# Performance work log

Measured on AMD Instinct MI355X. Metric: run time of the kernel, lower is better.

## Reference

```python
import jax, jax.numpy as jnp
from jax import lax
import numpy as np

CH = 512      # ch_in = c_in = c_out
P = 8         # p: channels per group
NG = CH // P  # depthwise groups
PG = CH // P  # pointwise groups
EPS = 1e-5
DN = ('NCHW', 'OIHW', 'NCHW')


def leaky(x):
    return jnp.where(x >= 0, x, 0.01 * x)  # LeakyReLU default slope


def setup_inputs() -> dict:
    key = jax.random.key(0)
    ks = jax.random.split(key, 8)
    N, H, W = 16, 64, 64
    return {
        'style_encoding': jax.random.normal(ks[0], (N, 512, 4, 4), jnp.float32),
        'content_in': jax.random.normal(ks[1], (N, CH, H, W), jnp.float32),
        'dw_w': jax.random.normal(ks[2], (P, 512, 2, 2), jnp.float32) * 0.05,
        'dw_b': jax.random.normal(ks[3], (P,), jnp.float32) * 0.05,
        'pk_w': jax.random.normal(ks[4], (P, 512), jnp.float32) * 0.05,
        'pk_b': jax.random.normal(ks[5], (P,), jnp.float32) * 0.05,
        'pb_w': jax.random.normal(ks[6], (CH, 512), jnp.float32) * 0.05,
        'pb_b': jax.random.normal(ks[7], (CH,), jnp.float32) * 0.05,
    }


def reference(style_encoding, content_in, dw_w, dw_b, pk_w, pk_b, pb_w, pb_b):
    N, _, H, W = content_in.shape
    # --- KernelPredictor ---
    # depthwise kernels: 2x2 valid conv on 4x4 style map -> [N, P, 3, 3]
    d = lax.conv_general_dilated(style_encoding, dw_w, (1, 1), 'VALID',
                                 dimension_numbers=DN)
    d = leaky(d + dw_b[None, :, None, None])  # [N, P, 3, 3]
    # expand: same [P,3,3] filter for every output channel -> [N, CH, P, 3, 3]
    depthwise = jnp.broadcast_to(d[:, None], (N, CH, P, 3, 3))
    # avg-pool 4 on 4x4 style map == global mean -> [N, 512]
    s_d = jnp.mean(style_encoding, axis=(2, 3))
    pk = jnp.einsum('nc,oc->no', s_d, pk_w) + pk_b       # [N, P]  (1x1 conv)
    bias = jnp.einsum('nc,oc->no', s_d, pb_w) + pb_b     # [N, CH] (1x1 conv)

    # --- per-sample grouped convs, batched by folding batch into groups ---
    padded = jnp.pad(content_in, ((0, 0), (0, 0), (1, 1), (1, 1)), mode='reflect')
    xr = padded.reshape(1, N * CH, H + 2, W + 2)
    wr = depthwise.reshape(N * CH, P, 3, 3)
    depth = lax.conv_general_dilated(xr, wr, (1, 1), 'VALID',
                                     feature_group_count=N * NG,
                                     dimension_numbers=DN)
    depth = depth.reshape(N, CH, H, W)

    # pointwise 1x1 grouped conv: weight [N, CH, P, 1, 1], identical over out
    # channels within a sample (expand); groups = PG, CH//PG == P out ch/group
    depth_g = depth.reshape(N, PG, P, H, W)
    pw_g = jnp.broadcast_to(pk[:, None, None, :], (N, PG, P, P))  # [n,g,o,j]
    out = jnp.einsum('ngjhw,ngoj->ngohw', depth_g, pw_g).reshape(N, CH, H, W)
    predicted = leaky(out + bias[:, :, None, None])

    # --- instance-norm of content (AdaIN calc_mean_std, unbiased var) ---
    mean = jnp.mean(content_in, axis=(2, 3), keepdims=True)
    std = jnp.sqrt(jnp.var(content_in, axis=(2, 3), keepdims=True, ddof=1) + EPS)
    normalized = (content_in - mean) / std
    return normalized * predicted
```

## Files before the change

### kernel.cpp

```cpp
#include <hip/hip_runtime.h>
#include <math.h>

#define CH 512
#define P 8
#define PLANE 4096
#define EPS 1e-5f

typedef float f4 __attribute__((ext_vector_type(4)));

__device__ __forceinline__ float leaky(float x) { return x >= 0.f ? x : 0.01f * x; }

__device__ __forceinline__ float wave_sum(float v) {
    #pragma unroll
    for (int off = 32; off; off >>= 1) v += __shfl_xor(v, off, 64);
    return v;
}

__global__ __launch_bounds__(64) void sd_pk_kernel(
    const float* __restrict__ style,
    const float* __restrict__ pk_w,
    const float* __restrict__ pk_b,
    float* __restrict__ sd_out,
    float* __restrict__ S_out)
{
    const int n = blockIdx.x;
    const int lane = threadIdx.x;
    const float4* sp = (const float4*)(style + (size_t)n * 8192);
    float sd[8];
    #pragma unroll
    for (int i = 0; i < 8; ++i) {
        int c = lane + 64 * i;
        float4 a = sp[c * 4 + 0], b = sp[c * 4 + 1];
        float4 d = sp[c * 4 + 2], e = sp[c * 4 + 3];
        float s = a.x + a.y + a.z + a.w + b.x + b.y + b.z + b.w
                + d.x + d.y + d.z + d.w + e.x + e.y + e.z + e.w;
        sd[i] = s * (1.f / 16.f);
        sd_out[n * 512 + c] = sd[i];
    }
    float Ssum = 0.f;
    #pragma unroll
    for (int o = 0; o < 8; ++o) {
        float acc = 0.f;
        #pragma unroll
        for (int i = 0; i < 8; ++i)
            acc += pk_w[o * 512 + lane + 64 * i] * sd[i];
        Ssum += wave_sum(acc) + pk_b[o];
    }
    if (lane == 0) S_out[n] = Ssum;
}

__global__ __launch_bounds__(256) void dconv_kernel(
    const float* __restrict__ style,
    const float* __restrict__ dw_w,
    const float* __restrict__ dw_b,
    float* __restrict__ d_pred)
{
    const int W = blockIdx.x * 4 + (threadIdx.x >> 6);
    const int lane = threadIdx.x & 63;
    const int n = W / 72, r = W % 72;
    const int j = r / 9, pos = r % 9, y = pos / 3, x = pos % 3;
    const float* sb = style + (size_t)n * 8192;
    const float4* wp = (const float4*)dw_w;
    float acc = 0.f;
    #pragma unroll
    for (int i = 0; i < 8; ++i) {
        int c = lane + 64 * i;
        float4 w = wp[j * 512 + c];
        const float* s = sb + c * 16 + y * 4 + x;
        acc += s[0] * w.x + s[1] * w.y + s[4] * w.z + s[5] * w.w;
    }
    acc = wave_sum(acc);
    if (lane == 0) d_pred[n * 72 + r] = leaky(acc + dw_b[j]);
}

__global__ __launch_bounds__(256) void bias_kernel(
    const float* __restrict__ sd,
    const float* __restrict__ pb_w,
    const float* __restrict__ pb_b,
    float* __restrict__ bias_out)
{
    const int c = blockIdx.x * 4 + (threadIdx.x >> 6);
    const int lane = threadIdx.x & 63;
    float w[8];
    #pragma unroll
    for (int i = 0; i < 8; ++i) w[i] = pb_w[(size_t)c * 512 + lane + 64 * i];
    float acc[16];
    #pragma unroll
    for (int nn = 0; nn < 16; ++nn) acc[nn] = 0.f;
    #pragma unroll
    for (int i = 0; i < 8; ++i) {
        #pragma unroll
        for (int nn = 0; nn < 16; ++nn)
            acc[nn] += w[i] * sd[nn * 512 + lane + 64 * i];
    }
    #pragma unroll
    for (int nn = 0; nn < 16; ++nn) acc[nn] = wave_sum(acc[nn]);
    if (lane == 0) {
        float bb = pb_b[c];
        #pragma unroll
        for (int nn = 0; nn < 16; ++nn) bias_out[nn * 512 + c] = acc[nn] + bb;
    }
}

__global__ __launch_bounds__(256) void stats_kernel(
    const float* __restrict__ content,
    float* __restrict__ mean_out,
    float* __restrict__ rstd_out)
{
    const int nc = blockIdx.x;
    const int t = threadIdx.x;
    const float4* base = (const float4*)(content + (size_t)nc * PLANE);
    float s = 0.f, sq = 0.f;
    #pragma unroll
    for (int k = 0; k < 4; ++k) {
        float4 v = base[k * 256 + t];
        s  += v.x + v.y + v.z + v.w;
        sq += v.x * v.x + v.y * v.y + v.z * v.z + v.w * v.w;
    }
    #pragma unroll
    for (int off = 32; off > 0; off >>= 1) {
        s  += __shfl_down(s, off, 64);
        sq += __shfl_down(sq, off, 64);
    }
    __shared__ float ls[4], lq[4];
    const int wave = t >> 6, lane = t & 63;
    if (lane == 0) { ls[wave] = s; lq[wave] = sq; }
    __syncthreads();
    if (t == 0) {
        float S = ls[0] + ls[1] + ls[2] + ls[3];
        float Q = lq[0] + lq[1] + lq[2] + lq[3];
        float m = S * (1.f / 4096.f);
        float var = (Q - 4096.f * m * m) * (1.f / 4095.f);
        mean_out[nc] = m;
        rstd_out[nc] = rsqrtf(var + EPS);
    }
}

__global__ __launch_bounds__(256) void main_kernel(
    const float* __restrict__ content,
    const float* __restrict__ d_pred,
    const float* __restrict__ S_in,
    const float* __restrict__ bias_in,
    const float* __restrict__ mean_in,
    const float* __restrict__ rstd_in,
    float* __restrict__ out)
{
    const int b    = blockIdx.x;
    const int tile = b & 3;
    const int g    = (b >> 2) & 63;
    const int n    = b >> 8;
    const int t  = threadIdx.x;
    const int tx = t & 15, ty = t >> 4;
    const int h  = tile * 16 + ty;
    const int x0 = tx * 4;

    __shared__ float s_d[72];
    __shared__ float s_S;
    __shared__ float s_bias[8], s_mean[8], s_rstd[8];
    if (t < 72) s_d[t] = d_pred[n * 72 + t];
    if (t == 80) s_S = S_in[n];
    if (t >= 88 && t < 96) {
        int o = t - 88;
        int c = n * 512 + g * 8 + o;
        s_bias[o] = bias_in[c];
        s_mean[o] = mean_in[c];
        s_rstd[o] = rstd_in[c];
    }
    __syncthreads();

    const float* cbase = content + (size_t)(n * 512 + g * 8) * PLANE;
    float D0 = 0.f, D1 = 0.f, D2 = 0.f, D3 = 0.f;
    float4 xc[8];

    #pragma unroll
    for (int j = 0; j < 8; ++j) {
        const float* cj = cbase + j * PLANE;
        #pragma unroll
        for (int r = 0; r < 3; ++r) {
            int y = h - 1 + r;
            int ry = y < 0 ? 1 : (y > 63 ? 62 : y);
            float4 v = *(const float4*)(cj + ry * 64 + x0);
            float lv = __shfl_up(v.w, 1, 64);
            float rv = __shfl_down(v.x, 1, 64);
            float xm = (tx == 0)  ? v.y : lv;
            float xp = (tx == 15) ? v.z : rv;
            const float w0 = s_d[j * 9 + r * 3 + 0];
            const float w1 = s_d[j * 9 + r * 3 + 1];
            const float w2 = s_d[j * 9 + r * 3 + 2];
            D0 += w0 * xm  + w1 * v.x + w2 * v.y;
            D1 += w0 * v.x + w1 * v.y + w2 * v.z;
            D2 += w0 * v.y + w1 * v.z + w2 * v.w;
            D3 += w0 * v.z + w1 * v.w + w2 * xp;
            if (r == 1) xc[j] = v;
        }
    }

    const float S = s_S;
    const float P0 = D0 * S, P1 = D1 * S, P2 = D2 * S, P3 = D3 * S;
    float* obase = out + (size_t)(n * 512 + g * 8) * PLANE + h * 64 + x0;
    #pragma unroll
    for (int o = 0; o < 8; ++o) {
        float bb = s_bias[o], m = s_mean[o], rs = s_rstd[o];
        f4 res;
        res.x = (xc[o].x - m) * rs * leaky(P0 + bb);
        res.y = (xc[o].y - m) * rs * leaky(P1 + bb);
        res.z = (xc[o].z - m) * rs * leaky(P2 + bb);
        res.w = (xc[o].w - m) * rs * leaky(P3 + bb);
        __builtin_nontemporal_store(res, (f4*)(obase + o * PLANE));
    }
}

extern "C" void kernel_launch(void* const* d_in, const int* in_sizes, int n_in,
                              void* d_out, int out_size, void* d_ws, size_t ws_size,
                              hipStream_t stream) {
    const float* style   = (const float*)d_in[0];
    const float* content = (const float*)d_in[1];
    const float* dw_w    = (const float*)d_in[2];
    const float* dw_b    = (const float*)d_in[3];
    const float* pk_w    = (const float*)d_in[4];
    const float* pk_b    = (const float*)d_in[5];
    const float* pb_w    = (const float*)d_in[6];
    const float* pb_b    = (const float*)d_in[7];
    float* out = (float*)d_out;
    float* ws  = (float*)d_ws;

    const int N = 16;
    float* sd_ws   = ws;
    float* d_pred  = sd_ws + N * 512;
    float* S_ws    = d_pred + N * 72;
    float* bias_ws = S_ws + N;
    float* mean_ws = bias_ws + N * 512;
    float* rstd_ws = mean_ws + N * 512;

    sd_pk_kernel<<<N, 64, 0, stream>>>(style, pk_w, pk_b, sd_ws, S_ws);
    dconv_kernel<<<N * 72 / 4, 256, 0, stream>>>(style, dw_w, dw_b, d_pred);
    bias_kernel<<<512 / 4, 256, 0, stream>>>(sd_ws, pb_w, pb_b, bias_ws);
    stats_kernel<<<N * 512, 256, 0, stream>>>(content, mean_ws, rstd_ws);
    main_kernel<<<N * 64 * 4, 256, 0, stream>>>(content, d_pred, S_ws, bias_ws,
                                                mean_ws, rstd_ws, out);
}
```

Measured before the change: 276.8 us.

## Fuse instance-norm statistics into main kernel with per-group blocks

Removes the separate stats kernel and computes per-channel mean and rstd inside the main kernel, with each block now covering a full 8-channel group across all four row tiles. The group's content is read once for statistics and then re-read for the convolution, with the re-read expected to hit cache instead of DRAM. The cost is four times fewer blocks and a serial tile loop per block, which lowers parallelism and latency hiding.

```diff
diff --git a/kernel.cpp b/kernel.cpp
--- a/kernel.cpp
+++ b/kernel.cpp
@@ -102,111 +102,100 @@
     }
 }
 
-__global__ __launch_bounds__(256) void stats_kernel(
-    const float* __restrict__ content,
-    float* __restrict__ mean_out,
-    float* __restrict__ rstd_out)
-{
-    const int nc = blockIdx.x;
-    const int t = threadIdx.x;
-    const float4* base = (const float4*)(content + (size_t)nc * PLANE);
-    float s = 0.f, sq = 0.f;
-    #pragma unroll
-    for (int k = 0; k < 4; ++k) {
-        float4 v = base[k * 256 + t];
-        s  += v.x + v.y + v.z + v.w;
-        sq += v.x * v.x + v.y * v.y + v.z * v.z + v.w * v.w;
-    }
-    #pragma unroll
-    for (int off = 32; off > 0; off >>= 1) {
-        s  += __shfl_down(s, off, 64);
-        sq += __shfl_down(sq, off, 64);
-    }
-    __shared__ float ls[4], lq[4];
-    const int wave = t >> 6, lane = t & 63;
-    if (lane == 0) { ls[wave] = s; lq[wave] = sq; }
-    __syncthreads();
-    if (t == 0) {
-        float S = ls[0] + ls[1] + ls[2] + ls[3];
-        float Q = lq[0] + lq[1] + lq[2] + lq[3];
-        float m = S * (1.f / 4096.f);
-        float var = (Q - 4096.f * m * m) * (1.f / 4095.f);
-        mean_out[nc] = m;
-        rstd_out[nc] = rsqrtf(var + EPS);
-    }
-}
-
 __global__ __launch_bounds__(256) void main_kernel(
     const float* __restrict__ content,
     const float* __restrict__ d_pred,
     const float* __restrict__ S_in,
     const float* __restrict__ bias_in,
-    const float* __restrict__ mean_in,
-    const float* __restrict__ rstd_in,
     float* __restrict__ out)
 {
-    const int b    = blockIdx.x;
-    const int tile = b & 3;
-    const int g    = (b >> 2) & 63;
-    const int n    = b >> 8;
+    const int b = blockIdx.x;
+    const int g = b & 63, n = b >> 6;
     const int t  = threadIdx.x;
     const int tx = t & 15, ty = t >> 4;
-    const int h  = tile * 16 + ty;
     const int x0 = tx * 4;
+    const int wave = t >> 6, lane = t & 63;
 
     __shared__ float s_d[72];
     __shared__ float s_S;
     __shared__ float s_bias[8], s_mean[8], s_rstd[8];
+
     if (t < 72) s_d[t] = d_pred[n * 72 + t];
     if (t == 80) s_S = S_in[n];
     if (t >= 88 && t < 96) {
         int o = t - 88;
-        int c = n * 512 + g * 8 + o;
-        s_bias[o] = bias_in[c];
-        s_mean[o] = mean_in[c];
-        s_rstd[o] = rstd_in[c];
+        s_bias[o] = bias_in[n * 512 + g * 8 + o];
+    }
+
+    const float* cbase = content + (size_t)(n * 512 + g * 8) * PLANE;
+
+    #pragma unroll
+    for (int jj = 0; jj < 2; ++jj) {
+        const int j = wave * 2 + jj;
+        const f4* p = (const f4*)(cbase + j * PLANE);
+        float s = 0.f, q = 0.f;
+        #pragma unroll 4
+        for (int k = 0; k < 16; ++k) {
+            f4 v = p[lane + 64 * k];
+            s += v.x + v.y + v.z + v.w;
+            q += v.x * v.x + v.y * v.y + v.z * v.z + v.w * v.w;
+        }
+        #pragma unroll
+        for (int off = 32; off; off >>= 1) {
+            s += __shfl_xor(s, off, 64);
+            q += __shfl_xor(q, off, 64);
+        }
+        if (lane == 0) {
+            float m = s * (1.f / 4096.f);
+            float var = (q - 4096.f * m * m) * (1.f / 4095.f);
+            s_mean[j] = m;
+            s_rstd[j] = rsqrtf(var + EPS);
+        }
     }
     __syncthreads();
 
-    const float* cbase = content + (size_t)(n * 512 + g * 8) * PLANE;
-    float D0 = 0.f, D1 = 0.f, D2 = 0.f, D3 = 0.f;
-    float4 xc[8];
-
-    #pragma unroll
-    for (int j = 0; j < 8; ++j) {
-        const float* cj = cbase + j * PLANE;
-        #pragma unroll
-        for (int r = 0; r < 3; ++r) {
-            int y = h - 1 + r;
-            int ry = y < 0 ? 1 : (y > 63 ? 62 : y);
-            float4 v = *(const float4*)(cj + ry * 64 + x0);
-            float lv = __shfl_up(v.w, 1, 64);
-            float rv = __shfl_down(v.x, 1, 64);
-            float xm = (tx == 0)  ? v.y : lv;
-            float xp = (tx == 15) ? v.z : rv;
-            const float w0 = s_d[j * 9 + r * 3 + 0];
-            const float w1 = s_d[j * 9 + r * 3 + 1];
-            const float w2 = s_d[j * 9 + r * 3 + 2];
-            D0 += w0 * xm  + w1 * v.x + w2 * v.y;
-            D1 += w0 * v.x + w1 * v.y + w2 * v.z;
-            D2 += w0 * v.y + w1 * v.z + w2 * v.w;
-            D3 += w0 * v.z + w1 * v.w + w2 * xp;
-            if (r == 1) xc[j] = v;
-        }
-    }
-
     const float S = s_S;
-    const float P0 = D0 * S, P1 = D1 * S, P2 = D2 * S, P3 = D3 * S;
-    float* obase = out + (size_t)(n * 512 + g * 8) * PLANE + h * 64 + x0;
-    #pragma unroll
-    for (int o = 0; o < 8; ++o) {
-        float bb = s_bias[o], m = s_mean[o], rs = s_rstd[o];
-        f4 res;
-        res.x = (xc[o].x - m) * rs * leaky(P0 + bb);
-        res.y = (xc[o].y - m) * rs * leaky(P1 + bb);
-        res.z = (xc[o].z - m) * rs * leaky(P2 + bb);
-        res.w = (xc[o].w - m) * rs * leaky(P3 + bb);
-        __builtin_nontemporal_store(res, (f4*)(obase + o * PLANE));
+    #pragma unroll 1
+    for (int tile = 0; tile < 4; ++tile) {
+        const int h = tile * 16 + ty;
+        float D0 = 0.f, D1 = 0.f, D2 = 0.f, D3 = 0.f;
+        float4 xc[8];
+
+        #pragma unroll
+        for (int j = 0; j < 8; ++j) {
+            const float* cj = cbase + j * PLANE;
+            #pragma unroll
+            for (int r = 0; r < 3; ++r) {
+                int y = h - 1 + r;
+                int ry = y < 0 ? 1 : (y > 63 ? 62 : y);
+                float4 v = *(const float4*)(cj + ry * 64 + x0);
+                float lv = __shfl_up(v.w, 1, 64);
+                float rv = __shfl_down(v.x, 1, 64);
+                float xm = (tx == 0)  ? v.y : lv;
+                float xp = (tx == 15) ? v.z : rv;
+                const float w0 = s_d[j * 9 + r * 3 + 0];
+                const float w1 = s_d[j * 9 + r * 3 + 1];
+                const float w2 = s_d[j * 9 + r * 3 + 2];
+                D0 += w0 * xm  + w1 * v.x + w2 * v.y;
+                D1 += w0 * v.x + w1 * v.y + w2 * v.z;
+                D2 += w0 * v.y + w1 * v.z + w2 * v.w;
+                D3 += w0 * v.z + w1 * v.w + w2 * xp;
+                if (r == 1) xc[j] = v;
+            }
+        }
+
+        const float P0 = D0 * S, P1 = D1 * S, P2 = D2 * S, P3 = D3 * S;
+        float* obase = out + (size_t)(n * 512 + g * 8) * PLANE + h * 64 + x0;
+        #pragma unroll
+        for (int o = 0; o < 8; ++o) {
+            float bb = s_bias[o], m = s_mean[o], rs = s_rstd[o];
+            f4 res;
+            res.x = (xc[o].x - m) * rs * leaky(P0 + bb);
+            res.y = (xc[o].y - m) * rs * leaky(P1 + bb);
+            res.z = (xc[o].z - m) * rs * leaky(P2 + bb);
+            res.w = (xc[o].w - m) * rs * leaky(P3 + bb);
+            __builtin_nontemporal_store(res, (f4*)(obase + o * PLANE));
+        }
     }
 }
 
@@ -229,13 +218,9 @@
     float* d_pred  = sd_ws + N * 512;
     float* S_ws    = d_pred + N * 72;
     float* bias_ws = S_ws + N;
-    float* mean_ws = bias_ws + N * 512;
-    float* rstd_ws = mean_ws + N * 512;
 
     sd_pk_kernel<<<N, 64, 0, stream>>>(style, pk_w, pk_b, sd_ws, S_ws);
     dconv_kernel<<<N * 72 / 4, 256, 0, stream>>>(style, dw_w, dw_b, d_pred);
     bias_kernel<<<512 / 4, 256, 0, stream>>>(sd_ws, pb_w, pb_b, bias_ws);
-    stats_kernel<<<N * 512, 256, 0, stream>>>(content, mean_ws, rstd_ws);
-    main_kernel<<<N * 64 * 4, 256, 0, stream>>>(content, d_pred, S_ws, bias_ws,
-                                                mean_ws, rstd_ws, out);
-}
+    main_kernel<<<N * 64, 256, 0, stream>>>(content, d_pred, S_ws, bias_ws, out);
+}
```

New measurement: 290.4 us. 1.05x slower.
